# Kernel optimization log

Hardware: AMD Instinct MI355X
Metric: run time of the kernel (lower is better)

## Reference

```python
import jax, jax.numpy as jnp
import numpy as np
import math

B, T, C = 4, 2048, 1024
H = 16
D = C // H

def setup_inputs() -> dict:
    key = jax.random.key(0)
    k1, k2, k3 = jax.random.split(key, 3)
    x = jax.random.normal(k1, (B, T, C), dtype=jnp.float32)
    w_attn = jax.random.normal(k2, (3 * C, C), dtype=jnp.float32) * (1.0 / math.sqrt(C))
    b_attn = jnp.zeros((3 * C,), dtype=jnp.float32)
    w_proj = jax.random.normal(k3, (C, C), dtype=jnp.float32) * (1.0 / math.sqrt(C))
    b_proj = jnp.zeros((C,), dtype=jnp.float32)
    return {"x": x, "w_attn": w_attn, "b_attn": b_attn, "w_proj": w_proj, "b_proj": b_proj}

def reference(x, w_attn, b_attn, w_proj, b_proj):
    Bq, Tq, Cq = x.shape
    qkv = x @ w_attn.T + b_attn                      # [B,T,3C]
    q, k, v = jnp.split(qkv, 3, axis=-1)
    q = q.reshape(Bq, Tq, H, D).transpose(0, 2, 1, 3)  # [B,H,T,D]
    k = k.reshape(Bq, Tq, H, D).transpose(0, 2, 1, 3)
    v = v.reshape(Bq, Tq, H, D).transpose(0, 2, 1, 3)
    att = jnp.einsum('bhqd,bhkd->bhqk', q, k) * (1.0 / math.sqrt(D))
    causal = jnp.tril(jnp.ones((Tq, Tq), dtype=bool))
    att = jnp.where(causal[None, None], att, -jnp.inf)
    att = jax.nn.softmax(att, axis=-1)
    y = jnp.einsum('bhqk,bhkd->bhqd', att, v)          # [B,H,T,D]
    y = y.transpose(0, 2, 1, 3).reshape(Bq, Tq, Cq)
    return y @ w_proj.T + b_proj
```

## Files before the change

kernel.cpp:

```cpp
#include <hip/hip_runtime.h>
#include <hip/hip_bf16.h>


typedef __hip_bfloat16 bf16;
typedef __attribute__((ext_vector_type(8))) short bf16x8;
typedef __attribute__((ext_vector_type(4))) float f32x4;
typedef __attribute__((ext_vector_type(16))) float f32x16;

#define MFMA16(a, b, c) __builtin_amdgcn_mfma_f32_16x16x32_bf16(a, b, c, 0, 0, 0)
#define MFMA32(a, b, c) __builtin_amdgcn_mfma_f32_32x32x16_bf16(a, b, c, 0, 0, 0)
#define GLOAD_LDS(g, l) __builtin_amdgcn_global_load_lds( \
    (const __attribute__((address_space(1))) void*)(g),    \
    (__attribute__((address_space(3))) void*)(l), 16, 0, 0)

constexpr int Bn = 4, Tn = 2048, Cn = 1024, Hn = 16, Dn = 64;
constexpr size_t HT_ELEMS = (size_t)64 * Tn * Dn;
constexpr float QSCALE = 0.18033688011112042f;

__device__ __forceinline__ short f2bf(float f) {
    unsigned u = __float_as_uint(f);
    return (short)((u + 0x7FFF + ((u >> 16) & 1)) >> 16);
}
__device__ __forceinline__ bf16 bfbits(short s) { bf16 b; __builtin_memcpy(&b, &s, 2); return b; }

__device__ __forceinline__ unsigned cvtpk_bf16(float lo, float hi) {
    unsigned r;
    asm("v_cvt_pk_bf16_f32 %0, %1, %2" : "=v"(r) : "v"(lo), "v"(hi));
    return r;
}
__device__ __forceinline__ void permswap(unsigned& a, unsigned& b) {
#if __has_builtin(__builtin_amdgcn_permlane32_swap)
    auto r = __builtin_amdgcn_permlane32_swap(a, b, false, false);
    a = (unsigned)r[0]; b = (unsigned)r[1];
#else
    asm("v_permlane32_swap_b32 %0, %1" : "+v"(a), "+v"(b));
#endif
}
__device__ __forceinline__ bf16x8 pack4(unsigned w0, unsigned w1, unsigned w2, unsigned w3) {
    union { unsigned u[4]; bf16x8 v; } t;
    t.u[0] = w0; t.u[1] = w1; t.u[2] = w2; t.u[3] = w3;
    return t.v;
}

__global__ __launch_bounds__(256) void cast3_kernel(
    const float* __restrict__ x, const float* __restrict__ wa,
    const float* __restrict__ wp, bf16* __restrict__ out)
{
    size_t i = (size_t)blockIdx.x * 256 + threadIdx.x;
    const float* src; size_t off;
    if (i < 1048576)      { src = x;  off = i; }
    else if (i < 1441792) { src = wa; off = i - 1048576; }
    else                  { src = wp; off = i - 1441792; }
    const float4* p = (const float4*)(src + off * 8);
    float4 a = p[0], b = p[1];
    bf16x8 r;
    r[0] = f2bf(a.x); r[1] = f2bf(a.y); r[2] = f2bf(a.z); r[3] = f2bf(a.w);
    r[4] = f2bf(b.x); r[5] = f2bf(b.y); r[6] = f2bf(b.z); r[7] = f2bf(b.w);
    *(bf16x8*)(out + i * 8) = r;
}

__global__ __launch_bounds__(512, 1) void qkv_gemm256(
    const bf16* __restrict__ Am, const bf16* __restrict__ Wm,
    const float* __restrict__ bias,
    bf16* __restrict__ qo, bf16* __restrict__ ko, bf16* __restrict__ vo)
{
    constexpr int K = 1024;
    __shared__ __align__(128) bf16 As[2][16384];
    __shared__ __align__(128) bf16 Bs[2][12288];
    const int tid  = threadIdx.x;
    const int lane = tid & 63;
    const int wid  = tid >> 6, wm = wid >> 2, wn = wid & 3;
    const int row16 = lane & 15, quad = lane >> 4;
    const unsigned bid = blockIdx.x;
    const int x8 = bid & 7, l = bid >> 3;
    const int tm = (x8 >> 1) * 8 + l / 8;
    const int tn = (x8 & 1) * 8 + l % 8;
    const int m0 = tm * 256, n0 = tn * 192;

    const int rL = tid >> 3;
    const int cS = (tid & 7) ^ (rL & 7);
    const char* Ab = (const char*)Am;
    const char* Bb = (const char*)Wm;
    const int axor = (row16 & 7) << 4;

    f32x4 acc[8][3];
    #pragma unroll
    for (int i = 0; i < 8; i++)
        #pragma unroll
        for (int j = 0; j < 3; j++) acc[i][j] = {0, 0, 0, 0};

#define STAGE_A(nb, k0) do {                                                    \
        _Pragma("unroll")                                                       \
        for (int g = 0; g < 4; g++)                                             \
            GLOAD_LDS(Ab + (size_t)(m0 + g * 64 + rL) * 2048 + (k0) * 2 + cS * 16, \
                      (char*)As[nb] + g * 8192 + tid * 16);                     \
    } while (0)
#define STAGE_B(nb, k0) do {                                                    \
        _Pragma("unroll")                                                       \
        for (int g = 0; g < 3; g++)                                             \
            GLOAD_LDS(Bb + (size_t)(n0 + g * 64 + rL) * 2048 + (k0) * 2 + cS * 16, \
                      (char*)Bs[nb] + g * 8192 + tid * 16);                     \
    } while (0)
#define DS_A(MQ, KK) do {                                                       \
        _Pragma("unroll")                                                       \
        for (int f = 0; f < 4; f++)                                             \
            aR[f] = *(const bf16x8*)(Ac + (wm * 128 + (MQ) * 64 + f * 16 + row16) * 128 \
                                        + (((KK) * 64 + quad * 16) ^ axor));    \
    } while (0)
#define DS_B(KK) do {                                                           \
        _Pragma("unroll")                                                       \
        for (int f = 0; f < 3; f++)                                             \
            bR[f] = *(const bf16x8*)(Bc + (wn * 48 + f * 16 + row16) * 128      \
                                        + (((KK) * 64 + quad * 16) ^ axor));    \
    } while (0)
#define MF12(MQ) do {                                                           \
        _Pragma("unroll")                                                       \
        for (int mf4 = 0; mf4 < 4; mf4++)                                       \
            _Pragma("unroll")                                                   \
            for (int nf = 0; nf < 3; nf++)                                      \
                acc[(MQ) * 4 + mf4][nf] = MFMA16(aR[mf4], bR[nf], acc[(MQ) * 4 + mf4][nf]); \
    } while (0)

    STAGE_A(0, 0);
    STAGE_B(0, 0);
    asm volatile("s_waitcnt vmcnt(0)" ::: "memory");
    __syncthreads();

    for (int t = 0; t < 16; ++t) {
        const int cur = t & 1, nxt = cur ^ 1;
        const char* Ac = (const char*)As[cur];
        const char* Bc = (const char*)Bs[cur];
        const int k1 = (t + 1) * 64;
        bf16x8 aR[4], bR[3];

        if (t < 15) STAGE_A(nxt, k1);
        DS_A(0, 0);
        DS_B(0);
        __builtin_amdgcn_s_barrier();
        asm volatile("s_waitcnt lgkmcnt(0)" ::: "memory");
        __builtin_amdgcn_sched_barrier(0);
        __builtin_amdgcn_s_setprio(1);  MF12(0);  __builtin_amdgcn_s_setprio(0);
        __builtin_amdgcn_s_barrier();

        if (t < 15) STAGE_B(nxt, k1);
        DS_A(1, 0);
        __builtin_amdgcn_s_barrier();
        asm volatile("s_waitcnt lgkmcnt(0)" ::: "memory");
        __builtin_amdgcn_sched_barrier(0);
        __builtin_amdgcn_s_setprio(1);  MF12(1);  __builtin_amdgcn_s_setprio(0);
        __builtin_amdgcn_s_barrier();

        DS_A(0, 1);
        DS_B(1);
        __builtin_amdgcn_s_barrier();
        asm volatile("s_waitcnt lgkmcnt(0)" ::: "memory");
        __builtin_amdgcn_sched_barrier(0);
        __builtin_amdgcn_s_setprio(1);  MF12(0);  __builtin_amdgcn_s_setprio(0);
        __builtin_amdgcn_s_barrier();

        DS_A(1, 1);
        __builtin_amdgcn_s_barrier();
        asm volatile("s_waitcnt lgkmcnt(0)" ::: "memory");
        __builtin_amdgcn_sched_barrier(0);
        __builtin_amdgcn_s_setprio(1);  MF12(1);  __builtin_amdgcn_s_setprio(0);
        asm volatile("s_waitcnt vmcnt(0)" ::: "memory");
        __builtin_amdgcn_s_barrier();
    }
#undef STAGE_A
#undef STAGE_B
#undef DS_A
#undef DS_B
#undef MF12

    #pragma unroll
    for (int mf = 0; mf < 8; mf++)
    #pragma unroll
    for (int nf = 0; nf < 3; nf++)
    #pragma unroll
    for (int r = 0; r < 4; r++) {
        int m = m0 + wm * 128 + mf * 16 + quad * 4 + r;
        int n = n0 + wn * 48 + nf * 16 + row16;
        float val = acc[mf][nf][r] + bias[n];
        int which = n >> 10, cc = n & 1023;
        if (which == 0) val *= QSCALE;
        bf16 bv = bfbits(f2bf(val));
        int h = cc >> 6, d = cc & 63;
        int b = m >> 11, t = m & 2047;
        int bh = b * Hn + h;
        if (which == 0)      qo[((size_t)bh * Tn + t) * Dn + d] = bv;
        else if (which == 1) ko[((size_t)bh * Tn + t) * Dn + d] = bv;
        else                 vo[((size_t)bh * Tn + t) * Dn + d] = bv;
    }
}

__global__ __launch_bounds__(256) void vtrans_kernel(
    const bf16* __restrict__ vr, bf16* __restrict__ vt)
{
    __shared__ bf16 T[32][72];
    const int tid = threadIdx.x;
    const int bh = blockIdx.x >> 6, kb = blockIdx.x & 63;
    const size_t base = ((size_t)bh * 64 + kb) * 2048;
    {
        const int t = tid >> 3, dch = tid & 7;
        bf16x8 v = *(const bf16x8*)(vr + base + t * 64 + dch * 8);
        *(bf16x8*)(&T[t][dch * 8]) = v;
    }
    __syncthreads();
    {
        const int d = tid >> 2, tkg = tid & 3;
        bf16x8 o;
        #pragma unroll
        for (int i = 0; i < 8; i++) o[i] = *(const short*)&T[tkg * 8 + i][d];
        *(bf16x8*)(vt + base + d * 32 + tkg * 8) = o;
    }
}

__global__ __launch_bounds__(256, 2) void attn_kernel(
    const bf16* __restrict__ qbp, const bf16* __restrict__ kbp,
    const bf16* __restrict__ vtb, bf16* __restrict__ ob)
{
    __shared__ __align__(128) bf16 SB[4][4096];
    __shared__ float lbufw[4][32];
    const int tid  = threadIdx.x;
    const int lane = tid & 63;
    const int w    = tid >> 6;
    const int l31  = lane & 31, hl = lane >> 5;
    const int bid  = blockIdx.x;
    const int qid  = bid & 7;
    const int idx  = bid >> 3;
    const int bh   = qid * 8 + (idx & 7);
    const int pair = idx >> 3;

    const int s2off = w * 2048 + (lane >> 3) * 128
                    + (((lane & 7) ^ ((lane >> 3) & 7)) << 4);
    const int kxor = (l31 & 7) << 4;
    const int sxor = ((l31 >> 1) & 7) << 4;

    const bf16* Q  = qbp + (size_t)bh * Tn * Dn;
    const char* Kh = (const char*)(kbp + (size_t)bh * Tn * Dn);
    const char* Vh = (const char*)vtb + (size_t)bh * 262144;

    #pragma unroll 1
    for (int sub = 0; sub < 2; sub++) {
        const int qb8   = sub ? (15 - pair) : pair;
        const int jmax2 = qb8 * 2 + 1;
        const int qtw   = qb8 * 4 + w;
        const int q0w   = qtw * 32;
        const int jd    = qtw >> 1;
        const int par   = qtw & 1;

        bf16x8 bQ[4];
        {
            const bf16* qp = Q + (size_t)(q0w + l31) * Dn + hl * 8;
            #pragma unroll
            for (int kf = 0; kf < 4; kf++) bQ[kf] = *(const bf16x8*)(qp + kf * 16);
        }

        f32x16 o2[2];
        o2[0] = {0,0,0,0,0,0,0,0,0,0,0,0,0,0,0,0};
        o2[1] = {0,0,0,0,0,0,0,0,0,0,0,0,0,0,0,0};
        float lsum = 0.f;

        GLOAD_LDS(Kh + s2off,        (char*)SB[0] + w * 2048);
        GLOAD_LDS(Kh + s2off + 1024, (char*)SB[0] + w * 2048 + 1024);
        GLOAD_LDS(Vh + s2off,        (char*)SB[2] + w * 2048);
        GLOAD_LDS(Vh + s2off + 1024, (char*)SB[2] + w * 2048 + 1024);
        __syncthreads();

        for (int j = 0; j <= jmax2; j++) {
            const int cur = j & 1;
            if (j < jmax2) {
                const int nb = cur ^ 1;
                const size_t go = (size_t)(j + 1) * 8192;
                GLOAD_LDS(Kh + go + s2off,        (char*)SB[nb] + w * 2048);
                GLOAD_LDS(Kh + go + s2off + 1024, (char*)SB[nb] + w * 2048 + 1024);
                GLOAD_LDS(Vh + go + s2off,        (char*)SB[2 + nb] + w * 2048);
                GLOAD_LDS(Vh + go + s2off + 1024, (char*)SB[2 + nb] + w * 2048 + 1024);
            }
            if (j <= jd) {
                const char* KB = (const char*)SB[cur];
                const char* VB = (const char*)SB[2 + cur];
                const bool doB = (j < jd) || par;

                bf16x8 aKa[4], aKb[4];
                #pragma unroll
                for (int kf = 0; kf < 4; kf++) {
                    const int co = ((kf * 2 + hl) << 4) ^ kxor;
                    aKa[kf] = *(const bf16x8*)(KB + l31 * 128 + co);
                    aKb[kf] = *(const bf16x8*)(KB + 4096 + l31 * 128 + co);
                }

                f32x16 sA = {0,0,0,0,0,0,0,0,0,0,0,0,0,0,0,0};
                f32x16 sB = {0,0,0,0,0,0,0,0,0,0,0,0,0,0,0,0};
                __builtin_amdgcn_s_setprio(1);
                #pragma unroll
                for (int kf = 0; kf < 4; kf++) sA = MFMA32(aKa[kf], bQ[kf], sA);
                if (doB) {
                    #pragma unroll
                    for (int kf = 0; kf < 4; kf++) sB = MFMA32(aKb[kf], bQ[kf], sB);
                }
                __builtin_amdgcn_s_setprio(0);

                bf16x8 vfL[4], vfH[4];
                #pragma unroll
                for (int i2 = 0; i2 < 4; i2++) {
                    const int vh = i2 >> 1, kc = i2 & 1;
                    const int off = (vh * 16 + (l31 >> 1)) * 128
                                  + ((((l31 & 1) * 4 + kc * 2 + hl) << 4) ^ sxor);
                    vfL[i2] = *(const bf16x8*)(VB + off);
                    if (doB) vfH[i2] = *(const bf16x8*)(VB + 4096 + off);
                }

                float pA[16];
                if (j == jd && par == 0) {
                    #pragma unroll
                    for (int r = 0; r < 16; r++) {
                        const int krow = (r & 3) + 8 * (r >> 2) + 4 * hl;
                        float e = exp2f(sA[r]);
                        pA[r] = (krow > l31) ? 0.f : e;
                    }
                } else {
                    #pragma unroll
                    for (int r = 0; r < 16; r++) pA[r] = exp2f(sA[r]);
                }
                lsum += (((pA[0]+pA[1]) + (pA[2]+pA[3])) + ((pA[4]+pA[5]) + (pA[6]+pA[7])))
                      + (((pA[8]+pA[9]) + (pA[10]+pA[11])) + ((pA[12]+pA[13]) + (pA[14]+pA[15])));

                unsigned a0 = cvtpk_bf16(pA[0],  pA[1]),  b0 = cvtpk_bf16(pA[4],  pA[5]);
                unsigned a1 = cvtpk_bf16(pA[2],  pA[3]),  b1 = cvtpk_bf16(pA[6],  pA[7]);
                unsigned a2 = cvtpk_bf16(pA[8],  pA[9]),  b2 = cvtpk_bf16(pA[12], pA[13]);
                unsigned a3 = cvtpk_bf16(pA[10], pA[11]), b3 = cvtpk_bf16(pA[14], pA[15]);
                permswap(a0, b0); permswap(a1, b1); permswap(a2, b2); permswap(a3, b3);
                const bf16x8 PA0 = pack4(a0, a1, b0, b1);
                const bf16x8 PA1 = pack4(a2, a3, b2, b3);

                __builtin_amdgcn_s_setprio(1);
                o2[0] = MFMA32(PA0, vfL[0], o2[0]);
                o2[0] = MFMA32(PA1, vfL[1], o2[0]);
                o2[1] = MFMA32(PA0, vfL[2], o2[1]);
                o2[1] = MFMA32(PA1, vfL[3], o2[1]);
                __builtin_amdgcn_s_setprio(0);

                if (doB) {
                    float pB[16];
                    if (j == jd) {
                        #pragma unroll
                        for (int r = 0; r < 16; r++) {
                            const int krow = (r & 3) + 8 * (r >> 2) + 4 * hl;
                            float e = exp2f(sB[r]);
                            pB[r] = (krow > l31) ? 0.f : e;
                        }
                    } else {
                        #pragma unroll
                        for (int r = 0; r < 16; r++) pB[r] = exp2f(sB[r]);
                    }
                    lsum += (((pB[0]+pB[1]) + (pB[2]+pB[3])) + ((pB[4]+pB[5]) + (pB[6]+pB[7])))
                          + (((pB[8]+pB[9]) + (pB[10]+pB[11])) + ((pB[12]+pB[13]) + (pB[14]+pB[15])));

                    unsigned c0_ = cvtpk_bf16(pB[0],  pB[1]),  d0_ = cvtpk_bf16(pB[4],  pB[5]);
                    unsigned c1_ = cvtpk_bf16(pB[2],  pB[3]),  d1_ = cvtpk_bf16(pB[6],  pB[7]);
                    unsigned c2_ = cvtpk_bf16(pB[8],  pB[9]),  d2_ = cvtpk_bf16(pB[12], pB[13]);
                    unsigned c3_ = cvtpk_bf16(pB[10], pB[11]), d3_ = cvtpk_bf16(pB[14], pB[15]);
                    permswap(c0_, d0_); permswap(c1_, d1_); permswap(c2_, d2_); permswap(c3_, d3_);
                    const bf16x8 PB0 = pack4(c0_, c1_, d0_, d1_);
                    const bf16x8 PB1 = pack4(c2_, c3_, d2_, d3_);

                    __builtin_amdgcn_s_setprio(1);
                    o2[0] = MFMA32(PB0, vfH[0], o2[0]);
                    o2[0] = MFMA32(PB1, vfH[1], o2[0]);
                    o2[1] = MFMA32(PB0, vfH[2], o2[1]);
                    o2[1] = MFMA32(PB1, vfH[3], o2[1]);
                    __builtin_amdgcn_s_setprio(0);
                }
            }
            __syncthreads();
        }

        unsigned lsu = __float_as_uint(lsum), lsv = lsu;
        permswap(lsu, lsv);
        const float ltot = __uint_as_float(lsu) + __uint_as_float(lsv);
        if (hl == 0) lbufw[w][l31] = 1.0f / ltot;
        asm volatile("s_waitcnt lgkmcnt(0)" ::: "memory");

        char* obl = (char*)SB[w];
        #pragma unroll
        for (int r = 0; r < 16; r++) {
            const int q  = (r & 3) + 8 * (r >> 2) + 4 * hl;
            const float rl = lbufw[w][q];
            const int qx = (q & 7) << 4;
            *(short*)(obl + q * 128 + ((2 * l31) ^ qx))      = f2bf(o2[0][r] * rl);
            *(short*)(obl + q * 128 + ((64 + 2 * l31) ^ qx)) = f2bf(o2[1][r] * rl);
        }
        asm volatile("s_waitcnt lgkmcnt(0)" ::: "memory");

        {
            const int q = lane >> 1, half = lane & 1;
            const int qx = (q & 7) << 4;
            const int b = bh >> 4, h = bh & 15;
            bf16* gdst = ob + ((size_t)(b * Tn + (q0w + q))) * Cn + h * Dn + half * 32;
            #pragma unroll
            for (int c = 0; c < 4; c++) {
                bf16x8 rv = *(const bf16x8*)(obl + q * 128 + (((half * 64) + c * 16) ^ qx));
                *(bf16x8*)(gdst + c * 8) = rv;
            }
        }
        __syncthreads();
    }
}

__global__ __launch_bounds__(256) void proj_gemm128(
    const bf16* __restrict__ Am, const bf16* __restrict__ Wm,
    const float* __restrict__ bias, float* __restrict__ out)
{
    constexpr int K = 1024;
    __shared__ bf16 As[4096], Bs[4096];
    const int tid = threadIdx.x;
    const int lane = tid & 63, w = tid >> 6;
    const int row = lane & 15, quad = lane >> 4;
    const unsigned bid = blockIdx.x;
    const int x8 = bid & 7, l = bid >> 3;
    const int tm = x8 * 8 + l / 8;
    const int tn = l % 8;
    const int m0 = tm * 128, n0 = tn * 128;

    const int srow = tid >> 2, skch = tid & 3;
    const bf16* ag0 = Am + (size_t)(m0 + srow) * K + skch * 8;
    const bf16* ag1 = ag0 + (size_t)64 * K;
    const bf16* wg0 = Wm + (size_t)(n0 + srow) * K + skch * 8;
    const bf16* wg1 = wg0 + (size_t)64 * K;
    bf16* asl0 = As + tid * 8;  bf16* asl1 = As + 2048 + tid * 8;
    bf16* bsl0 = Bs + tid * 8;  bf16* bsl1 = Bs + 2048 + tid * 8;

    f32x4 acc[4][4];
    #pragma unroll
    for (int i = 0; i < 4; i++)
        #pragma unroll
        for (int j = 0; j < 4; j++) acc[i][j] = {0, 0, 0, 0};

    const int r0 = (w >> 1) * 64, c0 = (w & 1) * 64;

    for (int k0 = 0; k0 < K; k0 += 32) {
        __syncthreads();
        GLOAD_LDS(ag0 + k0, asl0);
        GLOAD_LDS(ag1 + k0, asl1);
        GLOAD_LDS(wg0 + k0, bsl0);
        GLOAD_LDS(wg1 + k0, bsl1);
        __syncthreads();
        bf16x8 af[4], bfv[4];
        #pragma unroll
        for (int it = 0; it < 4; it++)
            af[it] = *(const bf16x8*)(As + (r0 + it * 16 + row) * 32 + quad * 8);
        #pragma unroll
        for (int jt = 0; jt < 4; jt++)
            bfv[jt] = *(const bf16x8*)(Bs + (c0 + jt * 16 + row) * 32 + quad * 8);
        #pragma unroll
        for (int it = 0; it < 4; it++)
            #pragma unroll
            for (int jt = 0; jt < 4; jt++)
                acc[it][jt] = MFMA16(af[it], bfv[jt], acc[it][jt]);
    }

    #pragma unroll
    for (int it = 0; it < 4; it++)
    #pragma unroll
    for (int jt = 0; jt < 4; jt++)
    #pragma unroll
    for (int r = 0; r < 4; r++) {
        int m = m0 + r0 + it * 16 + quad * 4 + r;
        int n = n0 + c0 + jt * 16 + row;
        out[(size_t)m * 1024 + n] = acc[it][jt][r] + bias[n];
    }
}

extern "C" void kernel_launch(void* const* d_in, const int* in_sizes, int n_in,
                              void* d_out, int out_size, void* d_ws, size_t ws_size,
                              hipStream_t stream) {
    const float* x      = (const float*)d_in[0];
    const float* w_attn = (const float*)d_in[1];
    const float* b_attn = (const float*)d_in[2];
    const float* w_proj = (const float*)d_in[3];
    const float* b_proj = (const float*)d_in[4];
    float* out = (float*)d_out;

    bf16* ws  = (bf16*)((char*)d_ws + 1024);
    bf16* xb  = ws;
    bf16* wab = xb  + (size_t)8192 * 1024;
    bf16* wpb = wab + (size_t)3072 * 1024;
    bf16* q   = wpb + (size_t)1024 * 1024;
    bf16* k   = q  + HT_ELEMS;
    bf16* vt  = k  + HT_ELEMS;
    bf16* o   = vt + HT_ELEMS;
    bf16* vrow = o;

    cast3_kernel<<<6144, 256, 0, stream>>>(x, w_attn, w_proj, xb);

    qkv_gemm256 <<<512, 512, 0, stream>>>(xb, wab, b_attn, q, k, vrow);
    vtrans_kernel<<<4096, 256, 0, stream>>>(vrow, vt);
    attn_kernel <<<512, 256, 0, stream>>>(q, k, vt, o);
    proj_gemm128<<<64 * 8, 256, 0, stream>>>(o, wpb, b_proj, out);
}
```

Before: 269.7 us.

## Replace double-buffered QKV GEMM pipeline with single-buffer loop and higher occupancy hint

Collapses the QKV GEMM's double-buffered LDS staging and its hand-interleaved barrier schedule into a single buffer. Each k-step now syncs, loads, syncs, then computes. The launch bound hint rises from 1 to 4 blocks per CU, so that other resident blocks can hide memory latency instead of software prefetch. The catch is that this removes the load/compute overlap inside each block, and the tighter register cap may force the 96-float accumulator tile to spill. LDS use per block (~56KB) also likely limits how many blocks can actually be resident.

```diff
diff --git a/kernel.cpp b/kernel.cpp
--- a/kernel.cpp
+++ b/kernel.cpp
@@ -59,14 +59,14 @@
     *(bf16x8*)(out + i * 8) = r;
 }
 
-__global__ __launch_bounds__(512, 1) void qkv_gemm256(
+__global__ __launch_bounds__(512, 4) void qkv_gemm256(
     const bf16* __restrict__ Am, const bf16* __restrict__ Wm,
     const float* __restrict__ bias,
     bf16* __restrict__ qo, bf16* __restrict__ ko, bf16* __restrict__ vo)
 {
     constexpr int K = 1024;
-    __shared__ __align__(128) bf16 As[2][16384];
-    __shared__ __align__(128) bf16 Bs[2][12288];
+    __shared__ __align__(128) bf16 As[16384];
+    __shared__ __align__(128) bf16 Bs[12288];
     const int tid  = threadIdx.x;
     const int lane = tid & 63;
     const int wid  = tid >> 6, wm = wid >> 2, wn = wid & 3;
@@ -89,29 +89,29 @@
         #pragma unroll
         for (int j = 0; j < 3; j++) acc[i][j] = {0, 0, 0, 0};
 
-#define STAGE_A(nb, k0) do {                                                    \
+#define STAGE_AB(k0) do {                                                       \
         _Pragma("unroll")                                                       \
         for (int g = 0; g < 4; g++)                                             \
             GLOAD_LDS(Ab + (size_t)(m0 + g * 64 + rL) * 2048 + (k0) * 2 + cS * 16, \
-                      (char*)As[nb] + g * 8192 + tid * 16);                     \
-    } while (0)
-#define STAGE_B(nb, k0) do {                                                    \
+                      (char*)As + g * 8192 + tid * 16);                         \
         _Pragma("unroll")                                                       \
         for (int g = 0; g < 3; g++)                                             \
             GLOAD_LDS(Bb + (size_t)(n0 + g * 64 + rL) * 2048 + (k0) * 2 + cS * 16, \
-                      (char*)Bs[nb] + g * 8192 + tid * 16);                     \
+                      (char*)Bs + g * 8192 + tid * 16);                         \
     } while (0)
 #define DS_A(MQ, KK) do {                                                       \
         _Pragma("unroll")                                                       \
         for (int f = 0; f < 4; f++)                                             \
-            aR[f] = *(const bf16x8*)(Ac + (wm * 128 + (MQ) * 64 + f * 16 + row16) * 128 \
-                                        + (((KK) * 64 + quad * 16) ^ axor));    \
+            aR[f] = *(const bf16x8*)((const char*)As                            \
+                        + (wm * 128 + (MQ) * 64 + f * 16 + row16) * 128         \
+                        + (((KK) * 64 + quad * 16) ^ axor));                    \
     } while (0)
 #define DS_B(KK) do {                                                           \
         _Pragma("unroll")                                                       \
         for (int f = 0; f < 3; f++)                                             \
-            bR[f] = *(const bf16x8*)(Bc + (wn * 48 + f * 16 + row16) * 128      \
-                                        + (((KK) * 64 + quad * 16) ^ axor));    \
+            bR[f] = *(const bf16x8*)((const char*)Bs                            \
+                        + (wn * 48 + f * 16 + row16) * 128                      \
+                        + (((KK) * 64 + quad * 16) ^ axor));                    \
     } while (0)
 #define MF12(MQ) do {                                                           \
         _Pragma("unroll")                                                       \
@@ -121,53 +121,19 @@
                 acc[(MQ) * 4 + mf4][nf] = MFMA16(aR[mf4], bR[nf], acc[(MQ) * 4 + mf4][nf]); \
     } while (0)
 
-    STAGE_A(0, 0);
-    STAGE_B(0, 0);
-    asm volatile("s_waitcnt vmcnt(0)" ::: "memory");
-    __syncthreads();
-
     for (int t = 0; t < 16; ++t) {
-        const int cur = t & 1, nxt = cur ^ 1;
-        const char* Ac = (const char*)As[cur];
-        const char* Bc = (const char*)Bs[cur];
-        const int k1 = (t + 1) * 64;
+        __syncthreads();
+        STAGE_AB(t * 64);
+        __syncthreads();
         bf16x8 aR[4], bR[3];
-
-        if (t < 15) STAGE_A(nxt, k1);
-        DS_A(0, 0);
-        DS_B(0);
-        __builtin_amdgcn_s_barrier();
-        asm volatile("s_waitcnt lgkmcnt(0)" ::: "memory");
-        __builtin_amdgcn_sched_barrier(0);
-        __builtin_amdgcn_s_setprio(1);  MF12(0);  __builtin_amdgcn_s_setprio(0);
-        __builtin_amdgcn_s_barrier();
-
-        if (t < 15) STAGE_B(nxt, k1);
-        DS_A(1, 0);
-        __builtin_amdgcn_s_barrier();
-        asm volatile("s_waitcnt lgkmcnt(0)" ::: "memory");
-        __builtin_amdgcn_sched_barrier(0);
-        __builtin_amdgcn_s_setprio(1);  MF12(1);  __builtin_amdgcn_s_setprio(0);
-        __builtin_amdgcn_s_barrier();
-
-        DS_A(0, 1);
-        DS_B(1);
-        __builtin_amdgcn_s_barrier();
-        asm volatile("s_waitcnt lgkmcnt(0)" ::: "memory");
-        __builtin_amdgcn_sched_barrier(0);
-        __builtin_amdgcn_s_setprio(1);  MF12(0);  __builtin_amdgcn_s_setprio(0);
-        __builtin_amdgcn_s_barrier();
-
-        DS_A(1, 1);
-        __builtin_amdgcn_s_barrier();
-        asm volatile("s_waitcnt lgkmcnt(0)" ::: "memory");
-        __builtin_amdgcn_sched_barrier(0);
-        __builtin_amdgcn_s_setprio(1);  MF12(1);  __builtin_amdgcn_s_setprio(0);
-        asm volatile("s_waitcnt vmcnt(0)" ::: "memory");
-        __builtin_amdgcn_s_barrier();
-    }
-#undef STAGE_A
-#undef STAGE_B
+        __builtin_amdgcn_s_setprio(1);
+        DS_A(0, 0); DS_B(0); MF12(0);
+        DS_A(1, 0);          MF12(1);
+        DS_A(0, 1); DS_B(1); MF12(0);
+        DS_A(1, 1);          MF12(1);
+        __builtin_amdgcn_s_setprio(0);
+    }
+#undef STAGE_AB
 #undef DS_A
 #undef DS_B
 #undef MF12
```

Result: faster. 250.4 us (-7.2%).
